# Kernel optimization log

Hardware: AMD Instinct MI355X
Metric: run time of the kernel (lower is better)

Reference implementation:

```python
import jax, jax.numpy as jnp
import numpy as np

N = 50000      # num nodes
E = 1600000    # num edges (before self-loops)
DIN, DH, DOUT = 256, 128, 64


def _gcn_norm(edge_index, num_nodes):
    # Add self-loops, then symmetric normalization 1/sqrt(deg_i * deg_j)
    loop = jnp.arange(num_nodes, dtype=edge_index.dtype)
    src = jnp.concatenate([edge_index[0], loop])  # [E+N]
    dst = jnp.concatenate([edge_index[1], loop])  # [E+N]
    deg = jax.ops.segment_sum(jnp.ones_like(dst, dtype=jnp.float32), dst,
                              num_segments=num_nodes)
    dinv = jnp.where(deg > 0, jax.lax.rsqrt(deg), 0.0)
    norm = dinv[src] * dinv[dst]  # [E+N]
    return src, dst, norm


def _gcn_conv(x, src, dst, norm, W, b, num_nodes):
    h = x @ W                                  # [N, out] dense transform first
    msg = h[src] * norm[:, None]               # gather + scale  [E+N, out]
    out = jax.ops.segment_sum(msg, dst, num_segments=num_nodes)  # scatter-add
    return out + b


def reference(x, edge_index, W1, b1, W2, b2):
    num_nodes = x.shape[0]
    src, dst, norm = _gcn_norm(edge_index, num_nodes)
    h = _gcn_conv(x, src, dst, norm, W1, b1, num_nodes)
    h = jax.nn.relu(h)
    # dropout(p=0.5) is identity in eval mode
    out = _gcn_conv(h, src, dst, norm, W2, b2, num_nodes)
    return out


def setup_inputs() -> dict:
    key = jax.random.key(0)
    ks = jax.random.split(key, 6)
    x = jax.random.normal(ks[0], (N, DIN), dtype=jnp.float32)
    edge_index = jax.random.randint(ks[1], (2, E), 0, N, dtype=jnp.int32)
    W1 = jax.random.normal(ks[2], (DIN, DH), dtype=jnp.float32) * (1.0 / np.sqrt(DIN))
    b1 = jnp.zeros((DH,), dtype=jnp.float32)
    W2 = jax.random.normal(ks[3], (DH, DOUT), dtype=jnp.float32) * (1.0 / np.sqrt(DH))
    b2 = jnp.zeros((DOUT,), dtype=jnp.float32)
    return {"x": x, "edge_index": edge_index, "W1": W1, "b1": b1, "W2": W2, "b2": b2}
```

## Files before the change

kernel.cpp:

```cpp
#include <hip/hip_runtime.h>

#define DIN 256
#define DH  128
#define DOUT 64
#define BSH  7
#define BNODES 128
#define MAXBUK 400
#define NBLK 512

typedef unsigned int  u32;
typedef unsigned short u16;
typedef __attribute__((ext_vector_type(8))) short bf16x8;
typedef __attribute__((ext_vector_type(4))) float f32x4;

__device__ inline u16 f2bf(float f) {
  u32 u = __float_as_uint(f);
  u32 r = u + 0x7FFF + ((u >> 16) & 1);
  return (u16)(r >> 16);
}
__device__ inline float bf2f_lo(u32 packed) { return __uint_as_float(packed << 16); }
__device__ inline float bf2f_hi(u32 packed) { return __uint_as_float(packed & 0xFFFF0000u); }


__global__ __launch_bounds__(256) void hist_kernel(const int* __restrict__ dst,
    int* __restrict__ counts, int E, int nbuk) {
  __shared__ int h[MAXBUK];
  int tid = threadIdx.x, b = blockIdx.x;
  for (int i = tid; i < nbuk; i += 256) h[i] = 0;
  __syncthreads();
  int ech = (E + NBLK - 1) / NBLK;
  int e0 = b * ech, e1 = min(E, e0 + ech);
  for (int e = e0 + tid; e < e1; e += 256)
    atomicAdd(&h[dst[e] >> BSH], 1);
  __syncthreads();
  for (int i = tid; i < nbuk; i += 256) counts[(size_t)i * NBLK + b] = h[i];
}

__global__ __launch_bounds__(256) void col_scan(int* __restrict__ counts,
    int* __restrict__ colsum, int nbuk) {
  __shared__ int sm[256];
  __shared__ int carry;
  int buk = blockIdx.x, t = threadIdx.x;
  if (t == 0) carry = 0;
  __syncthreads();
  int* row = counts + (size_t)buk * NBLK;
  for (int base = 0; base < NBLK; base += 256) {
    int v = row[base + t];
    sm[t] = v;
    __syncthreads();
    for (int d = 1; d < 256; d <<= 1) {
      int a = (t >= d) ? sm[t - d] : 0;
      __syncthreads();
      sm[t] += a;
      __syncthreads();
    }
    int excl = sm[t] - v + carry;
    row[base + t] = excl;
    __syncthreads();
    if (t == 255) carry = excl + v;
    __syncthreads();
  }
  if (t == 0) colsum[buk] = carry;
}

__global__ __launch_bounds__(256) void scan_block(int* partial, int* total_out, int nb, int n) {
  __shared__ int sm[256];
  __shared__ int carry;
  int t = threadIdx.x;
  if (t == 0) carry = 0;
  __syncthreads();
  for (int base = 0; base < nb; base += 256) {
    int g = base + t;
    int v = (g < nb) ? partial[g] : 0;
    sm[t] = v;
    __syncthreads();
    for (int d = 1; d < 256; d <<= 1) {
      int add = (t >= d) ? sm[t - d] : 0;
      __syncthreads();
      sm[t] += add;
      __syncthreads();
    }
    int excl = sm[t] - v + carry;
    if (g < nb) partial[g] = excl;
    __syncthreads();
    if (t == 255) carry = excl + v;
    __syncthreads();
  }
  if (t == 0) total_out[n] = carry;
}

__global__ __launch_bounds__(256) void scatter_kernel(const int* __restrict__ src,
    const int* __restrict__ dst, const int* __restrict__ counts,
    const int* __restrict__ bb, u32* __restrict__ ebuf, int E, int nbuk) {
  __shared__ int cur[MAXBUK];
  int tid = threadIdx.x, b = blockIdx.x;
  for (int i = tid; i < nbuk; i += 256)
    cur[i] = bb[i] + counts[(size_t)i * NBLK + b];
  __syncthreads();
  int ech = (E + NBLK - 1) / NBLK;
  int e0 = b * ech, e1 = min(E, e0 + ech);
  for (int e = e0 + tid; e < e1; e += 256) {
    int d = dst[e];
    int r = atomicAdd(&cur[d >> BSH], 1);
    ebuf[r] = (u32)src[e] | ((u32)(d & (BNODES - 1)) << 16);
  }
}

__global__ __launch_bounds__(256) void bucket_node_count(const u32* __restrict__ ebuf,
    const int* __restrict__ bb, int* __restrict__ cnt, int N) {
  __shared__ int c[BNODES];
  int b = blockIdx.x, tid = threadIdx.x;
  if (tid < BNODES) c[tid] = 0;
  __syncthreads();
  int e0 = bb[b], e1 = bb[b + 1];
  for (int e = e0 + tid; e < e1; e += 256)
    atomicAdd(&c[ebuf[e] >> 16], 1);
  __syncthreads();
  int node = b * BNODES + tid;
  if (tid < BNODES && node < N) cnt[node] = c[tid];
}

__global__ __launch_bounds__(256) void reduce_chunks(const int* __restrict__ cnt,
                                                     int* __restrict__ partial, int n) {
  int t = threadIdx.x;
  int g = blockIdx.x * 256 + t;
  int v = (g < n) ? cnt[g] : 0;
  #pragma unroll
  for (int o = 32; o > 0; o >>= 1) v += __shfl_down(v, o, 64);
  __shared__ int sm[4];
  if ((t & 63) == 0) sm[t >> 6] = v;
  __syncthreads();
  if (t == 0) partial[blockIdx.x] = sm[0] + sm[1] + sm[2] + sm[3];
}

__global__ __launch_bounds__(256) void scan_chunks(const int* __restrict__ cnt,
    const int* __restrict__ chunkoff, int* __restrict__ rowptr,
    float* __restrict__ dinv, int n) {
  __shared__ int sm[256];
  int t = threadIdx.x, g = blockIdx.x * 256 + t;
  int v = (g < n) ? cnt[g] : 0;
  sm[t] = v;
  __syncthreads();
  for (int d = 1; d < 256; d <<= 1) {
    int add = (t >= d) ? sm[t - d] : 0;
    __syncthreads();
    sm[t] += add;
    __syncthreads();
  }
  if (g < n) {
    rowptr[g] = sm[t] - v + chunkoff[blockIdx.x];
    dinv[g] = rsqrtf((float)(v + 1));
  }
}

__global__ __launch_bounds__(256) void bucket_fill(const u32* __restrict__ ebuf,
    const int* __restrict__ bb, const int* __restrict__ rowptr, int* __restrict__ csr) {
  __shared__ int c[BNODES];
  int b = blockIdx.x, tid = threadIdx.x;
  if (tid < BNODES) c[tid] = 0;
  __syncthreads();
  int e0 = bb[b], e1 = bb[b + 1];
  for (int e = e0 + tid; e < e1; e += 256) {
    u32 p = ebuf[e];
    int nl = p >> 16;
    int r = atomicAdd(&c[nl], 1);
    csr[rowptr[b * BNODES + nl] + r] = (int)(p & 0xFFFFu);
  }
}


__global__ __launch_bounds__(256) void w1_to_bf16T(const float* __restrict__ W1,
                                                   u16* __restrict__ w1t) {
  int t = blockIdx.x * 256 + threadIdx.x;
  int n = t >> 8, k = t & 255;
  w1t[t] = f2bf(W1[k * DH + n]);
}


__global__ __launch_bounds__(256) void gemm1_mfma(const float* __restrict__ x,
    const u16* __restrict__ w1t, const float* __restrict__ dinv,
    u16* __restrict__ h1, int M) {
  __shared__ u16 As[64][72];
  __shared__ u16 Bs[128][72];
  const int tid = threadIdx.x;
  const int lane = tid & 63, w = tid >> 6;
  const int row16 = lane & 15, quad = lane >> 4;
  const int rowBase = blockIdx.x * 64;
  f32x4 acc[8];
  #pragma unroll
  for (int nt = 0; nt < 8; ++nt) acc[nt] = (f32x4)(0.f);

  for (int kt = 0; kt < DIN; kt += 64) {
    {
      int r = tid >> 2, kq = tid & 3;
      int grow = rowBase + r;
      #pragma unroll
      for (int i = 0; i < 4; ++i) {
        float4 v = make_float4(0.f, 0.f, 0.f, 0.f);
        if (grow < M) v = *(const float4*)&x[(size_t)grow * DIN + kt + kq * 16 + i * 4];
        u32 lo = (u32)f2bf(v.x) | ((u32)f2bf(v.y) << 16);
        u32 hi = (u32)f2bf(v.z) | ((u32)f2bf(v.w) << 16);
        *(uint2*)&As[r][kq * 16 + i * 4] = make_uint2(lo, hi);
      }
    }
    {
      int n = tid >> 1, half = tid & 1;
      const uint4* s = (const uint4*)&w1t[n * DIN + kt + half * 32];
      uint4* d = (uint4*)&Bs[n][half * 32];
      d[0] = s[0]; d[1] = s[1]; d[2] = s[2]; d[3] = s[3];
    }
    __syncthreads();
    #pragma unroll
    for (int ks = 0; ks < 64; ks += 32) {
      bf16x8 a = *(bf16x8*)&As[w * 16 + row16][ks + quad * 8];
      #pragma unroll
      for (int nt = 0; nt < 8; ++nt) {
        bf16x8 b = *(bf16x8*)&Bs[nt * 16 + row16][ks + quad * 8];
        acc[nt] = __builtin_amdgcn_mfma_f32_16x16x32_bf16(a, b, acc[nt], 0, 0, 0);
      }
    }
    __syncthreads();
  }
  #pragma unroll
  for (int reg = 0; reg < 4; ++reg) {
    int row = rowBase + w * 16 + quad * 4 + reg;
    if (row < M) {
      float s = dinv[row];
      #pragma unroll
      for (int nt = 0; nt < 8; ++nt)
        h1[(size_t)row * DH + nt * 16 + row16] = f2bf(acc[nt][reg] * s);
    }
  }
}


template<int BN, int TN>
__global__ __launch_bounds__(256) void gemm_tile(const float* __restrict__ A,
    const float* __restrict__ W, const float* __restrict__ dinv,
    u16* __restrict__ C, int M, int K) {
  const int tid = threadIdx.x;
  const int tx = tid & 31;
  const int ty = tid >> 5;
  const int rowBase = blockIdx.x * 64;
  __shared__ float xs[64][16];
  __shared__ float wsm[16][BN];
  float acc[8][TN];
  #pragma unroll
  for (int r = 0; r < 8; ++r)
    #pragma unroll
    for (int j = 0; j < TN; ++j) acc[r][j] = 0.f;

  for (int kt = 0; kt < K; kt += 16) {
    {
      int r = tid >> 2, kq = tid & 3;
      int grow = rowBase + r;
      float4 v = make_float4(0.f, 0.f, 0.f, 0.f);
      if (grow < M) v = *(const float4*)&A[(size_t)grow * K + kt + kq * 4];
      *(float4*)&xs[r][kq * 4] = v;
    }
    #pragma unroll
    for (int i = 0; i < BN / 64; ++i) {
      int idx = (tid + i * 256) * 4;
      int kk = idx / BN, c = idx % BN;
      *(float4*)&wsm[kk][c] = *(const float4*)&W[(size_t)(kt + kk) * BN + c];
    }
    __syncthreads();
    #pragma unroll
    for (int kk = 0; kk < 16; ++kk) {
      float a[8];
      #pragma unroll
      for (int r = 0; r < 8; ++r) a[r] = xs[ty * 8 + r][kk];
      float b[TN];
      if (TN == 4) {
        float4 bv = *(float4*)&wsm[kk][tx * 4];
        b[0] = bv.x; b[1] = bv.y; b[2] = bv.z; b[3] = bv.w;
      } else {
        float2 bv = *(float2*)&wsm[kk][tx * 2];
        b[0] = bv.x; b[1] = bv.y;
      }
      #pragma unroll
      for (int r = 0; r < 8; ++r)
        #pragma unroll
        for (int j = 0; j < TN; ++j) acc[r][j] = fmaf(a[r], b[j], acc[r][j]);
    }
    __syncthreads();
  }
  #pragma unroll
  for (int r = 0; r < 8; ++r) {
    int row = rowBase + ty * 8 + r;
    if (row < M) {
      float s = dinv[row];
      if (TN == 4) {
        u32 lo = (u32)f2bf(acc[r][0] * s) | ((u32)f2bf(acc[r][1] * s) << 16);
        u32 hi = (u32)f2bf(acc[r][2] * s) | ((u32)f2bf(acc[r][3] * s) << 16);
        uint2 pv; pv.x = lo; pv.y = hi;
        *(uint2*)&C[(size_t)row * BN + tx * 4] = pv;
      } else {
        u32 lo = (u32)f2bf(acc[r][0] * s) | ((u32)f2bf(acc[r][1] * s) << 16);
        *(u32*)&C[(size_t)row * BN + tx * 2] = lo;
      }
    }
  }
}


__global__ __launch_bounds__(256) void aggregate1(const u16* __restrict__ h,
    const int* __restrict__ rowptr, const int* __restrict__ csr,
    const float* __restrict__ dinv, const float* __restrict__ bias,
    float* __restrict__ out, int n) {
  int lane = threadIdx.x & 63;
  int node = blockIdx.x * 4 + (threadIdx.x >> 6);
  if (node >= n) return;
  node = __builtin_amdgcn_readfirstlane(node);
  float di = dinv[node];
  int c0 = lane * 2;
  u32 w0 = *(const u32*)&h[(size_t)node * DH + c0];
  float ax = bf2f_lo(w0), ay = bf2f_hi(w0);
  int p = rowptr[node], pe = rowptr[node + 1];
  for (; p + 16 <= pe; p += 16) {
    int s[16];
    #pragma unroll
    for (int j = 0; j < 16; ++j) s[j] = csr[p + j];
    #pragma unroll
    for (int j = 0; j < 16; ++j) {
      u32 w = *(const u32*)&h[(size_t)s[j] * DH + c0];
      ax += bf2f_lo(w); ay += bf2f_hi(w);
    }
  }
  for (; p + 4 <= pe; p += 4) {
    int s[4];
    #pragma unroll
    for (int j = 0; j < 4; ++j) s[j] = csr[p + j];
    #pragma unroll
    for (int j = 0; j < 4; ++j) {
      u32 w = *(const u32*)&h[(size_t)s[j] * DH + c0];
      ax += bf2f_lo(w); ay += bf2f_hi(w);
    }
  }
  for (; p < pe; ++p) {
    u32 w = *(const u32*)&h[(size_t)csr[p] * DH + c0];
    ax += bf2f_lo(w); ay += bf2f_hi(w);
  }
  ax = fmaxf(fmaf(ax, di, bias[c0]), 0.f);
  ay = fmaxf(fmaf(ay, di, bias[c0 + 1]), 0.f);
  *(float2*)&out[(size_t)node * DH + c0] = make_float2(ax, ay);
}

__global__ __launch_bounds__(256) void aggregate2(const u16* __restrict__ h,
    const int* __restrict__ rowptr, const int* __restrict__ csr,
    const float* __restrict__ dinv, const float* __restrict__ bias,
    float* __restrict__ out, int n) {
  int lane = threadIdx.x & 63;
  int node = blockIdx.x * 4 + (threadIdx.x >> 6);
  if (node >= n) return;
  node = __builtin_amdgcn_readfirstlane(node);
  float di = dinv[node];
  float a = __uint_as_float((u32)h[(size_t)node * DOUT + lane] << 16);
  int p = rowptr[node], pe = rowptr[node + 1];
  for (; p + 16 <= pe; p += 16) {
    int s[16];
    #pragma unroll
    for (int j = 0; j < 16; ++j) s[j] = csr[p + j];
    #pragma unroll
    for (int j = 0; j < 16; ++j)
      a += __uint_as_float((u32)h[(size_t)s[j] * DOUT + lane] << 16);
  }
  for (; p + 4 <= pe; p += 4) {
    int s[4];
    #pragma unroll
    for (int j = 0; j < 4; ++j) s[j] = csr[p + j];
    #pragma unroll
    for (int j = 0; j < 4; ++j)
      a += __uint_as_float((u32)h[(size_t)s[j] * DOUT + lane] << 16);
  }
  for (; p < pe; ++p)
    a += __uint_as_float((u32)h[(size_t)csr[p] * DOUT + lane] << 16);
  out[(size_t)node * DOUT + lane] = fmaf(a, di, bias[lane]);
}


extern "C" void kernel_launch(void* const* d_in, const int* in_sizes, int n_in,
                              void* d_out, int out_size, void* d_ws, size_t ws_size,
                              hipStream_t stream) {
  const float* x  = (const float*)d_in[0];
  const int*   ei = (const int*)d_in[1];
  const float* W1 = (const float*)d_in[2];
  const float* b1 = (const float*)d_in[3];
  const float* W2 = (const float*)d_in[4];
  const float* b2 = (const float*)d_in[5];
  float* out = (float*)d_out;

  const int N = in_sizes[0] / DIN;
  const int E = in_sizes[1] / 2;
  const int* src = ei;
  const int* dst = ei + E;
  const int NB = (N + 255) / 256;
  const int nbuk = (N + BNODES - 1) / BNODES;

  char* ws = (char*)d_ws;
  size_t o = 0;
  auto alloc = [&](size_t bytes) { size_t r = o; o += (bytes + 511) & ~(size_t)511; return r; };
  size_t colsum_o  = alloc((size_t)(nbuk + 1) * 4);
  size_t counts_o  = alloc((size_t)nbuk * NBLK * 4);
  size_t rowptr_o  = alloc((size_t)(N + 1) * 4);
  size_t partial_o = alloc((size_t)NB * 4);
  size_t dinv_o    = alloc((size_t)N * 4);
  size_t cnt_o     = alloc((size_t)N * 4);
  size_t w1t_o     = alloc((size_t)DH * DIN * 2);
  size_t csr_o     = alloc((size_t)E * 4);
  size_t h1_o      = alloc((size_t)N * DH * 2);
  size_t g1_o      = alloc((size_t)N * DH * 4);
  size_t h2_o      = h1_o;
  size_t ebuf_o    = g1_o;

  int*   colsum  = (int*)(ws + colsum_o);
  int*   counts  = (int*)(ws + counts_o);
  int*   rowptr  = (int*)(ws + rowptr_o);
  int*   partial = (int*)(ws + partial_o);
  float* dinv    = (float*)(ws + dinv_o);
  int*   cnt     = (int*)(ws + cnt_o);
  u16*   w1t     = (u16*)(ws + w1t_o);
  int*   csr     = (int*)(ws + csr_o);
  u16*   h1      = (u16*)(ws + h1_o);
  float* g1      = (float*)(ws + g1_o);
  u16*   h2      = (u16*)(ws + h2_o);
  u32*   ebuf    = (u32*)(ws + ebuf_o);

  w1_to_bf16T<<<(DH * DIN) / 256, 256, 0, stream>>>(W1, w1t);
  hist_kernel<<<NBLK, 256, 0, stream>>>(dst, counts, E, nbuk);
  col_scan<<<nbuk, 256, 0, stream>>>(counts, colsum, nbuk);
  scan_block<<<1, 256, 0, stream>>>(colsum, colsum, nbuk, nbuk);
  scatter_kernel<<<NBLK, 256, 0, stream>>>(src, dst, counts, colsum, ebuf, E, nbuk);
  bucket_node_count<<<nbuk, 256, 0, stream>>>(ebuf, colsum, cnt, N);
  reduce_chunks<<<NB, 256, 0, stream>>>(cnt, partial, N);
  scan_block<<<1, 256, 0, stream>>>(partial, rowptr, NB, N);
  scan_chunks<<<NB, 256, 0, stream>>>(cnt, partial, rowptr, dinv, N);
  bucket_fill<<<nbuk, 256, 0, stream>>>(ebuf, colsum, rowptr, csr);

  gemm1_mfma<<<(N + 63) / 64, 256, 0, stream>>>(x, w1t, dinv, h1, N);
  aggregate1<<<(N + 3) / 4, 256, 0, stream>>>(h1, rowptr, csr, dinv, b1, g1, N);
  gemm_tile<DOUT, 2><<<(N + 63) / 64, 256, 0, stream>>>(g1, W2, dinv, h2, N, DH);
  aggregate2<<<(N + 3) / 4, 256, 0, stream>>>(h2, rowptr, csr, dinv, b2, out, N);
}
```

Before: 264.1 us.

## Split aggregation across feature chunks and edge groups with shuffle reduction

The two aggregation kernels are replaced by one templated kernel. Each wavefront now handles a single feature chunk of 16 columns for a node, and 8 lane groups each take a different neighbor edge in parallel. Partial sums are combined with cross-lane xor shuffles. This gives more independent gathers per wave and more blocks for average degree ~33. The cost is repeated csr/rowptr reads per chunk, an extra shuffle reduction, and short 32-byte gather segments per row.

```diff
diff --git a/kernel.cpp b/kernel.cpp
--- a/kernel.cpp
+++ b/kernel.cpp
@@ -304,78 +304,62 @@
 }
 
 
-__global__ __launch_bounds__(256) void aggregate1(const u16* __restrict__ h,
+template<int D, int LOGC, bool RELU>
+__global__ __launch_bounds__(256) void aggregate_k(const u16* __restrict__ h,
     const int* __restrict__ rowptr, const int* __restrict__ csr,
     const float* __restrict__ dinv, const float* __restrict__ bias,
     float* __restrict__ out, int n) {
-  int lane = threadIdx.x & 63;
-  int node = blockIdx.x * 4 + (threadIdx.x >> 6);
+  constexpr int NCH = 1 << LOGC;
+  constexpr int CW  = D / NCH;
+  constexpr int RS  = D / 2;
+  const u32* h32 = (const u32*)h;
+  int lane  = threadIdx.x & 63;
+  int chunk = blockIdx.x & (NCH - 1);
+  int node  = (blockIdx.x >> LOGC) * 4 + (threadIdx.x >> 6);
   if (node >= n) return;
   node = __builtin_amdgcn_readfirstlane(node);
+  int sub = lane & 7;
+  int eg  = lane >> 3;
+  int choff = chunk * (CW / 2);
   float di = dinv[node];
-  int c0 = lane * 2;
-  u32 w0 = *(const u32*)&h[(size_t)node * DH + c0];
-  float ax = bf2f_lo(w0), ay = bf2f_hi(w0);
+  float ax = 0.f, ay = 0.f;
+  if (eg == 0) {
+    u32 w = h32[(size_t)node * RS + choff + sub];
+    ax = bf2f_lo(w); ay = bf2f_hi(w);
+  }
   int p = rowptr[node], pe = rowptr[node + 1];
   for (; p + 16 <= pe; p += 16) {
-    int s[16];
-    #pragma unroll
-    for (int j = 0; j < 16; ++j) s[j] = csr[p + j];
-    #pragma unroll
-    for (int j = 0; j < 16; ++j) {
-      u32 w = *(const u32*)&h[(size_t)s[j] * DH + c0];
-      ax += bf2f_lo(w); ay += bf2f_hi(w);
-    }
-  }
-  for (; p + 4 <= pe; p += 4) {
-    int s[4];
-    #pragma unroll
-    for (int j = 0; j < 4; ++j) s[j] = csr[p + j];
-    #pragma unroll
-    for (int j = 0; j < 4; ++j) {
-      u32 w = *(const u32*)&h[(size_t)s[j] * DH + c0];
-      ax += bf2f_lo(w); ay += bf2f_hi(w);
-    }
-  }
-  for (; p < pe; ++p) {
-    u32 w = *(const u32*)&h[(size_t)csr[p] * DH + c0];
-    ax += bf2f_lo(w); ay += bf2f_hi(w);
-  }
-  ax = fmaxf(fmaf(ax, di, bias[c0]), 0.f);
-  ay = fmaxf(fmaf(ay, di, bias[c0 + 1]), 0.f);
-  *(float2*)&out[(size_t)node * DH + c0] = make_float2(ax, ay);
-}
-
-__global__ __launch_bounds__(256) void aggregate2(const u16* __restrict__ h,
-    const int* __restrict__ rowptr, const int* __restrict__ csr,
-    const float* __restrict__ dinv, const float* __restrict__ bias,
-    float* __restrict__ out, int n) {
-  int lane = threadIdx.x & 63;
-  int node = blockIdx.x * 4 + (threadIdx.x >> 6);
-  if (node >= n) return;
-  node = __builtin_amdgcn_readfirstlane(node);
-  float di = dinv[node];
-  float a = __uint_as_float((u32)h[(size_t)node * DOUT + lane] << 16);
-  int p = rowptr[node], pe = rowptr[node + 1];
-  for (; p + 16 <= pe; p += 16) {
-    int s[16];
-    #pragma unroll
-    for (int j = 0; j < 16; ++j) s[j] = csr[p + j];
-    #pragma unroll
-    for (int j = 0; j < 16; ++j)
-      a += __uint_as_float((u32)h[(size_t)s[j] * DOUT + lane] << 16);
-  }
-  for (; p + 4 <= pe; p += 4) {
-    int s[4];
-    #pragma unroll
-    for (int j = 0; j < 4; ++j) s[j] = csr[p + j];
-    #pragma unroll
-    for (int j = 0; j < 4; ++j)
-      a += __uint_as_float((u32)h[(size_t)s[j] * DOUT + lane] << 16);
-  }
-  for (; p < pe; ++p)
-    a += __uint_as_float((u32)h[(size_t)csr[p] * DOUT + lane] << 16);
-  out[(size_t)node * DOUT + lane] = fmaf(a, di, bias[lane]);
+    int s0 = csr[p + eg], s1 = csr[p + 8 + eg];
+    u32 w0 = h32[(size_t)s0 * RS + choff + sub];
+    u32 w1 = h32[(size_t)s1 * RS + choff + sub];
+    ax += bf2f_lo(w0) + bf2f_lo(w1);
+    ay += bf2f_hi(w0) + bf2f_hi(w1);
+  }
+  for (; p + 8 <= pe; p += 8) {
+    int s0 = csr[p + eg];
+    u32 w0 = h32[(size_t)s0 * RS + choff + sub];
+    ax += bf2f_lo(w0); ay += bf2f_hi(w0);
+  }
+  if (p < pe) {
+    u32 w0 = 0;
+    if (p + eg < pe) {
+      int s0 = csr[p + eg];
+      w0 = h32[(size_t)s0 * RS + choff + sub];
+    }
+    ax += bf2f_lo(w0); ay += bf2f_hi(w0);
+  }
+  #pragma unroll
+  for (int off = 8; off < 64; off <<= 1) {
+    ax += __shfl_xor(ax, off, 64);
+    ay += __shfl_xor(ay, off, 64);
+  }
+  if (eg == 0) {
+    int c0 = chunk * CW + sub * 2;
+    float fx = fmaf(ax, di, bias[c0]);
+    float fy = fmaf(ay, di, bias[c0 + 1]);
+    if (RELU) { fx = fmaxf(fx, 0.f); fy = fmaxf(fy, 0.f); }
+    *(float2*)&out[(size_t)node * D + c0] = make_float2(fx, fy);
+  }
 }
 
 
@@ -438,7 +422,7 @@
   bucket_fill<<<nbuk, 256, 0, stream>>>(ebuf, colsum, rowptr, csr);
 
   gemm1_mfma<<<(N + 63) / 64, 256, 0, stream>>>(x, w1t, dinv, h1, N);
-  aggregate1<<<(N + 3) / 4, 256, 0, stream>>>(h1, rowptr, csr, dinv, b1, g1, N);
+  aggregate_k<DH, 3, true><<<((N + 3) / 4) * 8, 256, 0, stream>>>(h1, rowptr, csr, dinv, b1, g1, N);
   gemm_tile<DOUT, 2><<<(N + 63) / 64, 256, 0, stream>>>(g1, W2, dinv, h2, N, DH);
-  aggregate2<<<(N + 3) / 4, 256, 0, stream>>>(h2, rowptr, csr, dinv, b2, out, N);
-}
+  aggregate_k<DOUT, 2, false><<<((N + 3) / 4) * 4, 256, 0, stream>>>(h2, rowptr, csr, dinv, b2, out, N);
+}
```

Result: slower. 453.5 us (+71.7%).

## Use bf16 MFMA for second GEMM and store aggregated layer-1 output as bf16

Applied to the files above, without the earlier changes.

Replaces the FP32 scalar tiled second GEMM with a bf16 MFMA kernel that stages the whole K=128 tile in shared memory. Layer-1 aggregation now writes bf16 instead of fp32, which halves the intermediate's memory traffic. W2 is transposed and converted to bf16 in a combined weight-prep kernel. This adds rounding error on the hidden activations before layer 2.

```diff
diff --git a/kernel.cpp b/kernel.cpp
--- a/kernel.cpp
+++ b/kernel.cpp
@@ -169,11 +169,17 @@
 }
 
 
-__global__ __launch_bounds__(256) void w1_to_bf16T(const float* __restrict__ W1,
-                                                   u16* __restrict__ w1t) {
+__global__ __launch_bounds__(256) void w_prep(const float* __restrict__ W1,
+    const float* __restrict__ W2, u16* __restrict__ w1t, u16* __restrict__ w2t) {
   int t = blockIdx.x * 256 + threadIdx.x;
-  int n = t >> 8, k = t & 255;
-  w1t[t] = f2bf(W1[k * DH + n]);
+  if (t < DH * DIN) {
+    int n = t >> 8, k = t & 255;
+    w1t[t] = f2bf(W1[k * DH + n]);
+  } else {
+    int t2 = t - DH * DIN;
+    int n = t2 >> 7, k = t2 & 127;
+    w2t[t2] = f2bf(W2[k * DOUT + n]);
+  }
 }
 
 
@@ -234,71 +240,52 @@
 }
 
 
-template<int BN, int TN>
-__global__ __launch_bounds__(256) void gemm_tile(const float* __restrict__ A,
-    const float* __restrict__ W, const float* __restrict__ dinv,
-    u16* __restrict__ C, int M, int K) {
+__global__ __launch_bounds__(256) void gemm2_mfma(const u16* __restrict__ g1,
+    const u16* __restrict__ w2t, const float* __restrict__ dinv,
+    u16* __restrict__ h2, int M) {
+  __shared__ u16 As[64][136];
+  __shared__ u16 Bs[64][136];
   const int tid = threadIdx.x;
-  const int tx = tid & 31;
-  const int ty = tid >> 5;
+  const int lane = tid & 63, w = tid >> 6;
+  const int row16 = lane & 15, quad = lane >> 4;
   const int rowBase = blockIdx.x * 64;
-  __shared__ float xs[64][16];
-  __shared__ float wsm[16][BN];
-  float acc[8][TN];
-  #pragma unroll
-  for (int r = 0; r < 8; ++r)
-    #pragma unroll
-    for (int j = 0; j < TN; ++j) acc[r][j] = 0.f;
-
-  for (int kt = 0; kt < K; kt += 16) {
-    {
-      int r = tid >> 2, kq = tid & 3;
-      int grow = rowBase + r;
-      float4 v = make_float4(0.f, 0.f, 0.f, 0.f);
-      if (grow < M) v = *(const float4*)&A[(size_t)grow * K + kt + kq * 4];
-      *(float4*)&xs[r][kq * 4] = v;
-    }
-    #pragma unroll
-    for (int i = 0; i < BN / 64; ++i) {
-      int idx = (tid + i * 256) * 4;
-      int kk = idx / BN, c = idx % BN;
-      *(float4*)&wsm[kk][c] = *(const float4*)&W[(size_t)(kt + kk) * BN + c];
-    }
-    __syncthreads();
-    #pragma unroll
-    for (int kk = 0; kk < 16; ++kk) {
-      float a[8];
-      #pragma unroll
-      for (int r = 0; r < 8; ++r) a[r] = xs[ty * 8 + r][kk];
-      float b[TN];
-      if (TN == 4) {
-        float4 bv = *(float4*)&wsm[kk][tx * 4];
-        b[0] = bv.x; b[1] = bv.y; b[2] = bv.z; b[3] = bv.w;
-      } else {
-        float2 bv = *(float2*)&wsm[kk][tx * 2];
-        b[0] = bv.x; b[1] = bv.y;
-      }
-      #pragma unroll
-      for (int r = 0; r < 8; ++r)
-        #pragma unroll
-        for (int j = 0; j < TN; ++j) acc[r][j] = fmaf(a[r], b[j], acc[r][j]);
-    }
-    __syncthreads();
-  }
-  #pragma unroll
-  for (int r = 0; r < 8; ++r) {
-    int row = rowBase + ty * 8 + r;
+  f32x4 acc[4];
+  #pragma unroll
+  for (int nt = 0; nt < 4; ++nt) acc[nt] = (f32x4)(0.f);
+
+  #pragma unroll
+  for (int i = 0; i < 4; ++i) {
+    int flat = i * 256 + tid;
+    int r = flat >> 4, c = flat & 15;
+    int grow = rowBase + r;
+    uint4 v = make_uint4(0, 0, 0, 0);
+    if (grow < M) v = *(const uint4*)&g1[(size_t)grow * DH + c * 8];
+    *(uint4*)&As[r][c * 8] = v;
+  }
+  #pragma unroll
+  for (int i = 0; i < 4; ++i) {
+    int flat = i * 256 + tid;
+    int r = flat >> 4, c = flat & 15;
+    *(uint4*)&Bs[r][c * 8] = *(const uint4*)&w2t[r * DH + c * 8];
+  }
+  __syncthreads();
+  #pragma unroll
+  for (int ks = 0; ks < 128; ks += 32) {
+    bf16x8 a = *(bf16x8*)&As[w * 16 + row16][ks + quad * 8];
+    #pragma unroll
+    for (int nt = 0; nt < 4; ++nt) {
+      bf16x8 b = *(bf16x8*)&Bs[nt * 16 + row16][ks + quad * 8];
+      acc[nt] = __builtin_amdgcn_mfma_f32_16x16x32_bf16(a, b, acc[nt], 0, 0, 0);
+    }
+  }
+  #pragma unroll
+  for (int reg = 0; reg < 4; ++reg) {
+    int row = rowBase + w * 16 + quad * 4 + reg;
     if (row < M) {
       float s = dinv[row];
-      if (TN == 4) {
-        u32 lo = (u32)f2bf(acc[r][0] * s) | ((u32)f2bf(acc[r][1] * s) << 16);
-        u32 hi = (u32)f2bf(acc[r][2] * s) | ((u32)f2bf(acc[r][3] * s) << 16);
-        uint2 pv; pv.x = lo; pv.y = hi;
-        *(uint2*)&C[(size_t)row * BN + tx * 4] = pv;
-      } else {
-        u32 lo = (u32)f2bf(acc[r][0] * s) | ((u32)f2bf(acc[r][1] * s) << 16);
-        *(u32*)&C[(size_t)row * BN + tx * 2] = lo;
-      }
+      #pragma unroll
+      for (int nt = 0; nt < 4; ++nt)
+        h2[(size_t)row * DOUT + nt * 16 + row16] = f2bf(acc[nt][reg] * s);
     }
   }
 }
@@ -307,7 +294,7 @@
 __global__ __launch_bounds__(256) void aggregate1(const u16* __restrict__ h,
     const int* __restrict__ rowptr, const int* __restrict__ csr,
     const float* __restrict__ dinv, const float* __restrict__ bias,
-    float* __restrict__ out, int n) {
+    u16* __restrict__ out, int n) {
   int lane = threadIdx.x & 63;
   int node = blockIdx.x * 4 + (threadIdx.x >> 6);
   if (node >= n) return;
@@ -343,7 +330,8 @@
   }
   ax = fmaxf(fmaf(ax, di, bias[c0]), 0.f);
   ay = fmaxf(fmaf(ay, di, bias[c0 + 1]), 0.f);
-  *(float2*)&out[(size_t)node * DH + c0] = make_float2(ax, ay);
+  u32 pk = (u32)f2bf(ax) | ((u32)f2bf(ay) << 16);
+  *(u32*)&out[(size_t)node * DH + c0] = pk;
 }
 
 __global__ __launch_bounds__(256) void aggregate2(const u16* __restrict__ h,
@@ -407,9 +395,10 @@
   size_t dinv_o    = alloc((size_t)N * 4);
   size_t cnt_o     = alloc((size_t)N * 4);
   size_t w1t_o     = alloc((size_t)DH * DIN * 2);
+  size_t w2t_o     = alloc((size_t)DOUT * DH * 2);
   size_t csr_o     = alloc((size_t)E * 4);
   size_t h1_o      = alloc((size_t)N * DH * 2);
-  size_t g1_o      = alloc((size_t)N * DH * 4);
+  size_t g1_o      = alloc((size_t)N * DH * 2);
   size_t h2_o      = h1_o;
   size_t ebuf_o    = g1_o;
 
@@ -420,13 +409,14 @@
   float* dinv    = (float*)(ws + dinv_o);
   int*   cnt     = (int*)(ws + cnt_o);
   u16*   w1t     = (u16*)(ws + w1t_o);
+  u16*   w2t     = (u16*)(ws + w2t_o);
   int*   csr     = (int*)(ws + csr_o);
   u16*   h1      = (u16*)(ws + h1_o);
-  float* g1      = (float*)(ws + g1_o);
+  u16*   g1      = (u16*)(ws + g1_o);
   u16*   h2      = (u16*)(ws + h2_o);
   u32*   ebuf    = (u32*)(ws + ebuf_o);
 
-  w1_to_bf16T<<<(DH * DIN) / 256, 256, 0, stream>>>(W1, w1t);
+  w_prep<<<(DH * DIN + DOUT * DH) / 256, 256, 0, stream>>>(W1, W2, w1t, w2t);
   hist_kernel<<<NBLK, 256, 0, stream>>>(dst, counts, E, nbuk);
   col_scan<<<nbuk, 256, 0, stream>>>(counts, colsum, nbuk);
   scan_block<<<1, 256, 0, stream>>>(colsum, colsum, nbuk, nbuk);
@@ -439,6 +429,6 @@
 
   gemm1_mfma<<<(N + 63) / 64, 256, 0, stream>>>(x, w1t, dinv, h1, N);
   aggregate1<<<(N + 3) / 4, 256, 0, stream>>>(h1, rowptr, csr, dinv, b1, g1, N);
-  gemm_tile<DOUT, 2><<<(N + 63) / 64, 256, 0, stream>>>(g1, W2, dinv, h2, N, DH);
+  gemm2_mfma<<<(N + 63) / 64, 256, 0, stream>>>(g1, w2t, dinv, h2, N);
   aggregate2<<<(N + 3) / 4, 256, 0, stream>>>(h2, rowptr, csr, dinv, b2, out, N);
 }
```

Result: faster. 248.1 us (-6.0%).
